# Kernel tuning notes

Measured on AMD Instinct MI355X. Metric: run time of the kernel, lower is better.

## Reference

```python
import jax, jax.numpy as jnp
import numpy as np

GS = 14           # group_size = (14, 14); N must equal GS*GS
NUM_HEADS = 4
DIM = 128
POS_DIM = (DIM // 4) // 4  # 8
EPS = 1e-5


def _ln(x, g, b):
    mu = x.mean(-1, keepdims=True)
    var = ((x - mu) ** 2).mean(-1, keepdims=True)
    return (x - mu) * jax.lax.rsqrt(var + EPS) * g + b


def setup_inputs() -> dict:
    key = jax.random.key(0)
    ks = jax.random.split(key, 20)
    B, N, C = 1024, GS * GS, DIM
    s = lambda fan: 1.0 / np.sqrt(fan)
    inp = {
        "x": jax.random.normal(ks[0], (B, N, C), jnp.float32),
        # linear weights stored as [in, out] (torch W.T)
        "wq": jax.random.normal(ks[1], (C, C), jnp.float32) * s(C),
        "wkv": jax.random.normal(ks[2], (C, 2 * C), jnp.float32) * s(C),
        "wproj": jax.random.normal(ks[3], (C, C), jnp.float32) * s(C),
        "bproj": jnp.zeros((C,), jnp.float32),
        "pp_w": jax.random.normal(ks[4], (2, POS_DIM), jnp.float32) * s(2),
        "pp_b": jnp.zeros((POS_DIM,), jnp.float32),
        "ln1_g": jnp.ones((POS_DIM,), jnp.float32),
        "ln1_b": jnp.zeros((POS_DIM,), jnp.float32),
        "l1_w": jax.random.normal(ks[5], (POS_DIM, POS_DIM), jnp.float32) * s(POS_DIM),
        "l1_b": jnp.zeros((POS_DIM,), jnp.float32),
        "ln2_g": jnp.ones((POS_DIM,), jnp.float32),
        "ln2_b": jnp.zeros((POS_DIM,), jnp.float32),
        "l2_w": jax.random.normal(ks[6], (POS_DIM, POS_DIM), jnp.float32) * s(POS_DIM),
        "l2_b": jnp.zeros((POS_DIM,), jnp.float32),
        "ln3_g": jnp.ones((POS_DIM,), jnp.float32),
        "ln3_b": jnp.zeros((POS_DIM,), jnp.float32),
        "l3_w": jax.random.normal(ks[7], (POS_DIM, NUM_HEADS), jnp.float32) * s(POS_DIM),
        "l3_b": jnp.zeros((NUM_HEADS,), jnp.float32),
    }
    return inp


def _rel_pos_index():
    # relative_position_index for square window (len(group_size)==2 branch)
    ch = jnp.arange(GS)
    coords = jnp.stack(jnp.meshgrid(ch, ch, indexing="ij"))        # [2, GS, GS]
    cf = coords.reshape(2, -1)                                       # [2, N]
    rel = cf[:, :, None] - cf[:, None, :]                            # [2, N, N]
    rel = rel.transpose(1, 2, 0)                                     # [N, N, 2]
    rel = rel + jnp.array([GS - 1, GS - 1])
    idx = rel[..., 0] * (2 * GS - 1) + rel[..., 1]                   # [N, N]
    return idx


def _biases():
    p = jnp.arange(1 - GS, GS)
    b = jnp.stack(jnp.meshgrid(p, p, indexing="ij"))                 # [2, 2GS-1, 2GS-1]
    return b.reshape(2, -1).T.astype(jnp.float32)                    # [(2GS-1)^2, 2]


def reference(x, wq, wkv, wproj, bproj, pp_w, pp_b,
              ln1_g, ln1_b, l1_w, l1_b,
              ln2_g, ln2_b, l2_w, l2_b,
              ln3_g, ln3_b, l3_w, l3_b):
    B, N, C = x.shape
    H = NUM_HEADS
    hd = C // H
    scale = hd ** -0.5

    q = (x @ wq).reshape(B, N, H, hd).transpose(0, 2, 1, 3)          # [B,H,N,hd]
    kv = (x @ wkv).reshape(B, N, 2, H, hd)
    k = kv[:, :, 0].transpose(0, 2, 1, 3)                            # [B,H,N,hd]
    v = kv[:, :, 1].transpose(0, 2, 1, 3)

    attn = jnp.einsum("bhqd,bhkd->bhqk", q, k) * scale               # [B,H,N,N]

    # dynamic position bias: tiny MLP over relative coords, residual=False path
    pos = _biases() @ pp_w + pp_b                                    # [M, pos_dim]
    pos = jax.nn.relu(_ln(pos, ln1_g, ln1_b)) @ l1_w + l1_b
    pos = jax.nn.relu(_ln(pos, ln2_g, ln2_b)) @ l2_w + l2_b
    pos = jax.nn.relu(_ln(pos, ln3_g, ln3_b)) @ l3_w + l3_b          # [M, H]

    rpb = pos[_rel_pos_index()]                                      # [N,N,H] gather
    attn = attn + rpb.transpose(2, 0, 1)[None]                       # [B,H,N,N]

    attn = jax.nn.softmax(attn, axis=-1)
    out = jnp.einsum("bhqk,bhkd->bhqd", attn, v)                     # [B,H,N,hd]
    out = out.transpose(0, 2, 1, 3).reshape(B, N, C)
    return out @ wproj + bproj
```

## Files before the change

kernel.cpp:

```cpp
#include <hip/hip_runtime.h>

typedef __attribute__((ext_vector_type(8))) __bf16 bf16x8;
typedef __attribute__((ext_vector_type(4))) __bf16 bf16x4;
typedef __attribute__((ext_vector_type(4))) float f32x4;
typedef __attribute__((ext_vector_type(4))) short s16x4;

#define MFMA32(a,b,c) __builtin_amdgcn_mfma_f32_16x16x32_bf16(a, b, c, 0, 0, 0)

static __device__ inline f32x4 MFMAX16(s16x4 a, s16x4 b, f32x4 c) {
#if __has_builtin(__builtin_amdgcn_mfma_f32_16x16x16bf16_1k)
  return __builtin_amdgcn_mfma_f32_16x16x16bf16_1k(a, b, c, 0, 0, 0);
#else
  f32x4 d;
  asm("v_mfma_f32_16x16x16_bf16 %0, %1, %2, %3" : "=v"(d) : "v"(a), "v"(b), "v"(c));
  return d;
#endif
}

#define KS 36
#define VS 212
#define NW 4

__device__ inline bf16x8 load_a_f32(const float* p) {
  const float4* q = (const float4*)p;
  float4 u = q[0], v = q[1];
  bf16x8 r;
  r[0] = (__bf16)u.x; r[1] = (__bf16)u.y; r[2] = (__bf16)u.z; r[3] = (__bf16)u.w;
  r[4] = (__bf16)v.x; r[5] = (__bf16)v.y; r[6] = (__bf16)v.z; r[7] = (__bf16)v.w;
  return r;
}

__device__ inline void lnrelu8(float* v, const float* g, const float* bta) {
  float mu = 0.f;
#pragma unroll
  for (int i = 0; i < 8; i++) mu += v[i];
  mu *= 0.125f;
  float var = 0.f;
#pragma unroll
  for (int i = 0; i < 8; i++) { float d = v[i] - mu; var += d * d; }
  var *= 0.125f;
  float inv = rsqrtf(var + 1e-5f);
#pragma unroll
  for (int i = 0; i < 8; i++) v[i] = fmaxf((v[i] - mu) * inv * g[i] + bta[i], 0.f);
}

__global__ void k_prep(const float* __restrict__ wq, const float* __restrict__ wkv,
                       const float* __restrict__ wproj,
                       const float* __restrict__ pp_w, const float* __restrict__ pp_b,
                       const float* ln1_g, const float* ln1_b, const float* l1_w, const float* l1_b,
                       const float* ln2_g, const float* ln2_b, const float* l2_w, const float* l2_b,
                       const float* ln3_g, const float* ln3_b, const float* l3_w, const float* l3_b,
                       __bf16* __restrict__ wF, __bf16* __restrict__ wpT,
                       __bf16* __restrict__ biasT) {
  __shared__ float pos_s[4 * 729];
  int blk = blockIdx.x, tid = threadIdx.x;
  if (blk < 88) {
    int t = blk * 256 + tid;
    if (t < 6144) {
      int lane = t & 63, frag = t >> 6;
      int kc = frag & 3, nt = (frag >> 2) & 1, tt = (frag >> 3) % 3, h = frag / 24;
      int col = lane & 15, quad = lane >> 4;
      int o = h * 32 + nt * 16 + col;
      int ibase = kc * 32 + quad * 8;
      bf16x8 vv;
#pragma unroll
      for (int j = 0; j < 8; j++) {
        int in = ibase + j;
        float w = (tt == 0) ? wq[in * 128 + o]
                : (tt == 1) ? wkv[in * 256 + o]
                            : wkv[in * 256 + 128 + o];
        vv[j] = (__bf16)w;
      }
      *(bf16x8*)&wF[(size_t)t * 8] = vv;
    } else if (t < 6144 + 16384) {
      int t2 = t - 6144;
      int o = t2 >> 7, i = t2 & 127;
      wpT[t2] = (__bf16)wproj[i * 128 + o];
    }
    return;
  }
  for (int m = tid; m < 729; m += 256) {
    float dr = (float)(m / 27) - 13.f, dc = (float)(m % 27) - 13.f;
    float a[8], bv[8];
#pragma unroll
    for (int j = 0; j < 8; j++) a[j] = dr * pp_w[j] + dc * pp_w[8 + j] + pp_b[j];
    lnrelu8(a, ln1_g, ln1_b);
#pragma unroll
    for (int o = 0; o < 8; o++) {
      float s = l1_b[o];
#pragma unroll
      for (int j = 0; j < 8; j++) s += a[j] * l1_w[j * 8 + o];
      bv[o] = s;
    }
    lnrelu8(bv, ln2_g, ln2_b);
#pragma unroll
    for (int o = 0; o < 8; o++) {
      float s = l2_b[o];
#pragma unroll
      for (int j = 0; j < 8; j++) s += bv[j] * l2_w[j * 8 + o];
      a[o] = s;
    }
    lnrelu8(a, ln3_g, ln3_b);
#pragma unroll
    for (int o = 0; o < 4; o++) {
      float s = l3_b[o];
#pragma unroll
      for (int j = 0; j < 8; j++) s += a[j] * l3_w[j * 4 + o];
      pos_s[o * 729 + m] = s;
    }
  }
  __syncthreads();
  int t = (blk - 88) * 256 + tid;
  int g = t % 52; int rem = t / 52; int qi = rem % 208; int h = rem / 208;
  int kj0 = g * 4;
  int r1 = qi / 14, c1 = qi % 14;
  bf16x4 o;
#pragma unroll
  for (int r = 0; r < 4; r++) {
    int kj = kj0 + r;
    float v = 0.f;
    if (qi < 196 && kj < 196) {
      int r2 = kj / 14, c2 = kj % 14;
      v = pos_s[h * 729 + (r1 - r2 + 13) * 27 + (c1 - c2 + 13)];
    }
    o[r] = (__bf16)v;
  }
  *(bf16x4*)&biasT[((size_t)(h * 208 + qi)) * 208 + kj0] = o;
}

__launch_bounds__(256, 4)
__global__ void k_attn(const float* __restrict__ x, const __bf16* __restrict__ wF,
                       const __bf16* __restrict__ biasT, __bf16* __restrict__ Og) {
  __shared__ __align__(16) __bf16 k_s[208 * KS];
  __shared__ __align__(16) __bf16 vT_s[32 * VS];

  int tid = threadIdx.x;
  int wv = tid >> 6, lane = tid & 63, col = lane & 15, quad = lane >> 4;
  int bi = blockIdx.x;
  int b = (bi & 7) * 128 + (bi >> 5);
  int h = (bi >> 3) & 3;

  const __bf16* wH = wF + (size_t)h * 12288;
#define WG(t, nt, kc) (*(const bf16x8*)&wH[(((t) * 2 + (nt)) * 4 + (kc)) * 512 + lane * 8])

  const float* xb = x + (size_t)b * (196 * 128);
  const float scale = 0.17677669529663687f;

  s16x4 qb[4][2];

#pragma unroll
  for (int i = 0; i < 4; i++) {
    int qt = wv + i * NW;
    if (qt < 13) {
      int row = qt * 16 + col;
      const float* ap = xb + (size_t)(row < 196 ? row : 0) * 128 + quad * 8;
      bf16x8 xf[4];
#pragma unroll
      for (int kc = 0; kc < 4; kc++) xf[kc] = load_a_f32(ap + kc * 32);
#pragma unroll
      for (int nt = 0; nt < 2; nt++) {
        f32x4 acc = {0.f, 0.f, 0.f, 0.f};
#pragma unroll
        for (int kc = 0; kc < 4; kc++) acc = MFMA32(WG(1, nt, kc), xf[kc], acc);
        bf16x4 pk;
#pragma unroll
        for (int r = 0; r < 4; r++) pk[r] = (__bf16)acc[r];
        *(bf16x4*)&k_s[row * KS + nt * 16 + quad * 4] = pk;
      }
#pragma unroll
      for (int nt = 0; nt < 2; nt++) {
        f32x4 acc = {0.f, 0.f, 0.f, 0.f};
#pragma unroll
        for (int kc = 0; kc < 4; kc++) acc = MFMA32(xf[kc], WG(2, nt, kc), acc);
        bf16x4 pk;
#pragma unroll
        for (int r = 0; r < 4; r++) pk[r] = (__bf16)acc[r];
        *(bf16x4*)&vT_s[(nt * 16 + col) * VS + qt * 16 + quad * 4] = pk;
      }
#pragma unroll
      for (int nt = 0; nt < 2; nt++) {
        f32x4 acc = {0.f, 0.f, 0.f, 0.f};
#pragma unroll
        for (int kc = 0; kc < 4; kc++) acc = MFMA32(WG(0, nt, kc), xf[kc], acc);
        bf16x4 pk;
#pragma unroll
        for (int r = 0; r < 4; r++) pk[r] = (__bf16)(acc[r] * scale);
        qb[i][nt] = __builtin_bit_cast(s16x4, pk);
      }
    }
  }
  __syncthreads();

#pragma unroll
  for (int i = 0; i < 4; i++) {
    int qt = wv + i * NW;
    if (qt < 13) {
      int qi = qt * 16 + col;
      const __bf16* brow = biasT + ((size_t)(h * 208 + qi)) * 208 + quad * 4;
      bf16x4 bl[13];
#pragma unroll
      for (int kt = 0; kt < 13; kt++) bl[kt] = *(const bf16x4*)(brow + kt * 16);

      float sum = 0.f;
      s16x4 pp[13];
#pragma unroll
      for (int kt = 0; kt < 13; kt++) {
        s16x4 ka0 = *(const s16x4*)&k_s[(kt * 16 + col) * KS + quad * 4];
        s16x4 ka1 = *(const s16x4*)&k_s[(kt * 16 + col) * KS + 16 + quad * 4];
        f32x4 acc = {0.f, 0.f, 0.f, 0.f};
        acc = MFMAX16(ka0, qb[i][0], acc);
        acc = MFMAX16(ka1, qb[i][1], acc);
        bf16x4 pk;
#pragma unroll
        for (int r = 0; r < 4; r++) {
          float e = __expf(acc[r] + (float)bl[kt][r]);
          if (kt == 12 && quad != 0) e = 0.f;
          sum += e;
          pk[r] = (__bf16)e;
        }
        pp[kt] = __builtin_bit_cast(s16x4, pk);
      }
      sum += __shfl_xor(sum, 16);
      sum += __shfl_xor(sum, 32);
      float inv = 1.f / sum;

      f32x4 o0a = {0.f,0.f,0.f,0.f}, o0b = {0.f,0.f,0.f,0.f};
      f32x4 o1a = {0.f,0.f,0.f,0.f}, o1b = {0.f,0.f,0.f,0.f};
#pragma unroll
      for (int kt = 0; kt < 13; kt++) {
        s16x4 va0 = *(const s16x4*)&vT_s[col * VS + kt * 16 + quad * 4];
        s16x4 va1 = *(const s16x4*)&vT_s[(16 + col) * VS + kt * 16 + quad * 4];
        if (kt & 1) { o0b = MFMAX16(va0, pp[kt], o0b); o1b = MFMAX16(va1, pp[kt], o1b); }
        else        { o0a = MFMAX16(va0, pp[kt], o0a); o1a = MFMAX16(va1, pp[kt], o1a); }
      }
      if (qi < 196) {
        __bf16* og = Og + ((size_t)b * 196 + qi) * 128 + h * 32;
        bf16x4 s0, s1;
#pragma unroll
        for (int r = 0; r < 4; r++) {
          s0[r] = (__bf16)((o0a[r] + o0b[r]) * inv);
          s1[r] = (__bf16)((o1a[r] + o1b[r]) * inv);
        }
        *(bf16x4*)&og[quad * 4]      = s0;
        *(bf16x4*)&og[16 + quad * 4] = s1;
      }
    }
  }
#undef WG
}

__launch_bounds__(256, 4)
__global__ void k_proj(const __bf16* __restrict__ Og, const __bf16* __restrict__ wpT,
                       const float* __restrict__ bproj, float* __restrict__ out) {
  int tid = threadIdx.x, wv = tid >> 6, lane = tid & 63, col = lane & 15, quad = lane >> 4;
  size_t rb = (size_t)blockIdx.x * 64 + wv * 16;
  const __bf16* arow = Og + (rb + col) * 128 + quad * 8;
  bf16x8 af[4];
#pragma unroll
  for (int kc = 0; kc < 4; kc++) af[kc] = *(const bf16x8*)(arow + kc * 32);
#pragma unroll
  for (int nt = 0; nt < 8; nt++) {
    f32x4 acc = {0.f, 0.f, 0.f, 0.f};
#pragma unroll
    for (int kc = 0; kc < 4; kc++)
      acc = MFMA32(*(const bf16x8*)&wpT[(size_t)(nt * 16 + col) * 128 + kc * 32 + quad * 8],
                   af[kc], acc);
    int od = nt * 16 + quad * 4;
    float4 bp = *(const float4*)&bproj[od];
    float4 st = { acc[0] + bp.x, acc[1] + bp.y, acc[2] + bp.z, acc[3] + bp.w };
    *(float4*)&out[(rb + col) * 128 + od] = st;
  }
}

extern "C" void kernel_launch(void* const* d_in, const int* in_sizes, int n_in,
                              void* d_out, int out_size, void* d_ws, size_t ws_size,
                              hipStream_t stream) {
  const float* x     = (const float*)d_in[0];
  const float* wq    = (const float*)d_in[1];
  const float* wkv   = (const float*)d_in[2];
  const float* wproj = (const float*)d_in[3];
  const float* bproj = (const float*)d_in[4];
  const float* pp_w  = (const float*)d_in[5];
  const float* pp_b  = (const float*)d_in[6];
  const float* ln1_g = (const float*)d_in[7];
  const float* ln1_b = (const float*)d_in[8];
  const float* l1_w  = (const float*)d_in[9];
  const float* l1_b  = (const float*)d_in[10];
  const float* ln2_g = (const float*)d_in[11];
  const float* ln2_b = (const float*)d_in[12];
  const float* l2_w  = (const float*)d_in[13];
  const float* l2_b  = (const float*)d_in[14];
  const float* ln3_g = (const float*)d_in[15];
  const float* ln3_b = (const float*)d_in[16];
  const float* l3_w  = (const float*)d_in[17];
  const float* l3_b  = (const float*)d_in[18];
  float* out = (float*)d_out;

  char* ws = (char*)d_ws;
  __bf16* wF    = (__bf16*)ws;
  __bf16* wpT   = (__bf16*)(ws + 98304);
  __bf16* biasT = (__bf16*)(ws + 131072);
  __bf16* Og    = (__bf16*)(ws + 477184);

  k_prep<<<257, 256, 0, stream>>>(wq, wkv, wproj, pp_w, pp_b,
                                  ln1_g, ln1_b, l1_w, l1_b,
                                  ln2_g, ln2_b, l2_w, l2_b,
                                  ln3_g, ln3_b, l3_w, l3_b,
                                  wF, wpT, biasT);
  k_attn<<<4096, 256, 0, stream>>>(x, wF, biasT, Og);
  k_proj<<<3136, 256, 0, stream>>>(Og, wpT, bproj, out);
}
```

Baseline: 383.8 us.

## Use exp2 with prescaled logits, repack bias contiguously, double rows per proj block

Folds log2(e) into the query scale and into the precomputed relative-position bias so the softmax can call the hardware exp2 directly. The bias table is repacked so each lane reads its 13 bias quads from a contiguous 52-element run, which should make those loads more coalesced. The attention kernel's occupancy hint becomes a waves-per-EU attribute instead of the launch-bounds minimum. The projection kernel now handles 128 rows per block, so each weight load feeds two MFMAs; this halves the grid but raises register use.

```diff
diff --git a/kernel.cpp b/kernel.cpp
--- a/kernel.cpp
+++ b/kernel.cpp
@@ -20,6 +20,7 @@
 #define KS 36
 #define VS 212
 #define NW 4
+#define LOG2E 1.4426950408889634f
 
 __device__ inline bf16x8 load_a_f32(const float* p) {
   const float4* q = (const float4*)p;
@@ -51,7 +52,7 @@
                        const float* ln2_g, const float* ln2_b, const float* l2_w, const float* l2_b,
                        const float* ln3_g, const float* ln3_b, const float* l3_w, const float* l3_b,
                        __bf16* __restrict__ wF, __bf16* __restrict__ wpT,
-                       __bf16* __restrict__ biasT) {
+                       __bf16* __restrict__ biasP) {
   __shared__ float pos_s[4 * 729];
   int blk = blockIdx.x, tid = threadIdx.x;
   if (blk < 88) {
@@ -112,6 +113,7 @@
   __syncthreads();
   int t = (blk - 88) * 256 + tid;
   int g = t % 52; int rem = t / 52; int qi = rem % 208; int h = rem / 208;
+  int kt = g >> 2, qd = g & 3;
   int kj0 = g * 4;
   int r1 = qi / 14, c1 = qi % 14;
   bf16x4 o;
@@ -123,14 +125,15 @@
       int r2 = kj / 14, c2 = kj % 14;
       v = pos_s[h * 729 + (r1 - r2 + 13) * 27 + (c1 - c2 + 13)];
     }
-    o[r] = (__bf16)v;
-  }
-  *(bf16x4*)&biasT[((size_t)(h * 208 + qi)) * 208 + kj0] = o;
-}
-
-__launch_bounds__(256, 4)
+    o[r] = (__bf16)(v * LOG2E);
+  }
+  *(bf16x4*)&biasP[(((size_t)h * 208 + qi) * 4 + qd) * 52 + kt * 4] = o;
+}
+
+__launch_bounds__(256)
+__attribute__((amdgpu_waves_per_eu(4, 4)))
 __global__ void k_attn(const float* __restrict__ x, const __bf16* __restrict__ wF,
-                       const __bf16* __restrict__ biasT, __bf16* __restrict__ Og) {
+                       const __bf16* __restrict__ biasP, __bf16* __restrict__ Og) {
   __shared__ __align__(16) __bf16 k_s[208 * KS];
   __shared__ __align__(16) __bf16 vT_s[32 * VS];
 
@@ -144,7 +147,7 @@
 #define WG(t, nt, kc) (*(const bf16x8*)&wH[(((t) * 2 + (nt)) * 4 + (kc)) * 512 + lane * 8])
 
   const float* xb = x + (size_t)b * (196 * 128);
-  const float scale = 0.17677669529663687f;
+  const float scale = 0.17677669529663687f * LOG2E;
 
   s16x4 qb[4][2];
 
@@ -196,10 +199,10 @@
     int qt = wv + i * NW;
     if (qt < 13) {
       int qi = qt * 16 + col;
-      const __bf16* brow = biasT + ((size_t)(h * 208 + qi)) * 208 + quad * 4;
+      const __bf16* bp = biasP + (((size_t)h * 208 + qi) * 4 + quad) * 52;
       bf16x4 bl[13];
 #pragma unroll
-      for (int kt = 0; kt < 13; kt++) bl[kt] = *(const bf16x4*)(brow + kt * 16);
+      for (int kt = 0; kt < 13; kt++) bl[kt] = *(const bf16x4*)(bp + kt * 4);
 
       float sum = 0.f;
       s16x4 pp[13];
@@ -213,7 +216,7 @@
         bf16x4 pk;
 #pragma unroll
         for (int r = 0; r < 4; r++) {
-          float e = __expf(acc[r] + (float)bl[kt][r]);
+          float e = __builtin_amdgcn_exp2f(acc[r] + (float)bl[kt][r]);
           if (kt == 12 && quad != 0) e = 0.f;
           sum += e;
           pk[r] = (__bf16)e;
@@ -253,22 +256,30 @@
 __global__ void k_proj(const __bf16* __restrict__ Og, const __bf16* __restrict__ wpT,
                        const float* __restrict__ bproj, float* __restrict__ out) {
   int tid = threadIdx.x, wv = tid >> 6, lane = tid & 63, col = lane & 15, quad = lane >> 4;
-  size_t rb = (size_t)blockIdx.x * 64 + wv * 16;
-  const __bf16* arow = Og + (rb + col) * 128 + quad * 8;
-  bf16x8 af[4];
-#pragma unroll
-  for (int kc = 0; kc < 4; kc++) af[kc] = *(const bf16x8*)(arow + kc * 32);
+  size_t rb = (size_t)blockIdx.x * 128 + wv * 16;
+  const __bf16* arow0 = Og + (rb + col) * 128 + quad * 8;
+  const __bf16* arow1 = arow0 + (size_t)64 * 128;
+  bf16x8 af0[4], af1[4];
+#pragma unroll
+  for (int kc = 0; kc < 4; kc++) {
+    af0[kc] = *(const bf16x8*)(arow0 + kc * 32);
+    af1[kc] = *(const bf16x8*)(arow1 + kc * 32);
+  }
 #pragma unroll
   for (int nt = 0; nt < 8; nt++) {
-    f32x4 acc = {0.f, 0.f, 0.f, 0.f};
-#pragma unroll
-    for (int kc = 0; kc < 4; kc++)
-      acc = MFMA32(*(const bf16x8*)&wpT[(size_t)(nt * 16 + col) * 128 + kc * 32 + quad * 8],
-                   af[kc], acc);
+    f32x4 acc0 = {0.f, 0.f, 0.f, 0.f}, acc1 = {0.f, 0.f, 0.f, 0.f};
+#pragma unroll
+    for (int kc = 0; kc < 4; kc++) {
+      bf16x8 w = *(const bf16x8*)&wpT[(size_t)(nt * 16 + col) * 128 + kc * 32 + quad * 8];
+      acc0 = MFMA32(w, af0[kc], acc0);
+      acc1 = MFMA32(w, af1[kc], acc1);
+    }
     int od = nt * 16 + quad * 4;
     float4 bp = *(const float4*)&bproj[od];
-    float4 st = { acc[0] + bp.x, acc[1] + bp.y, acc[2] + bp.z, acc[3] + bp.w };
-    *(float4*)&out[(rb + col) * 128 + od] = st;
+    float4 st0 = { acc0[0] + bp.x, acc0[1] + bp.y, acc0[2] + bp.z, acc0[3] + bp.w };
+    float4 st1 = { acc1[0] + bp.x, acc1[1] + bp.y, acc1[2] + bp.z, acc1[3] + bp.w };
+    *(float4*)&out[(rb + col) * 128 + od] = st0;
+    *(float4*)&out[(rb + 64 + col) * 128 + od] = st1;
   }
 }
 
@@ -299,14 +310,14 @@
   char* ws = (char*)d_ws;
   __bf16* wF    = (__bf16*)ws;
   __bf16* wpT   = (__bf16*)(ws + 98304);
-  __bf16* biasT = (__bf16*)(ws + 131072);
+  __bf16* biasP = (__bf16*)(ws + 131072);
   __bf16* Og    = (__bf16*)(ws + 477184);
 
   k_prep<<<257, 256, 0, stream>>>(wq, wkv, wproj, pp_w, pp_b,
                                   ln1_g, ln1_b, l1_w, l1_b,
                                   ln2_g, ln2_b, l2_w, l2_b,
                                   ln3_g, ln3_b, l3_w, l3_b,
-                                  wF, wpT, biasT);
-  k_attn<<<4096, 256, 0, stream>>>(x, wF, biasT, Og);
-  k_proj<<<3136, 256, 0, stream>>>(Og, wpT, bproj, out);
-}
+                                  wF, wpT, biasP);
+  k_attn<<<4096, 256, 0, stream>>>(x, wF, biasP, Og);
+  k_proj<<<1568, 256, 0, stream>>>(Og, wpT, bproj, out);
+}
```

Result: faster. 365.2 us (-4.9%).
